# Optimization experiments

Hardware: AMD Instinct MI355X
Metric: run time of the kernel (lower is better)

## Reference

```python
import jax, jax.numpy as jnp
import numpy as np

B = 1024          # global batch
D = 512           # embedding_size
C = 100000        # num_classes (sum over 8 shards)
S = 64.0          # ArcFace scale
M = 0.5           # ArcFace additive angular margin
EPS = 1e-30


def setup_inputs() -> dict:
    key = jax.random.key(0)
    k1, k2, k3 = jax.random.split(key, 3)
    embeddings = jax.random.normal(k1, (B, D), dtype=jnp.float32)
    weight = jax.random.normal(k2, (C, D), dtype=jnp.float32)
    labels = jax.random.randint(k3, (B,), 0, C, dtype=jnp.int64)
    return {"embeddings": embeddings, "weight": weight, "labels": labels}


def reference(embeddings, weight, labels):
    # normalize(embeddings), normalize(weight) -> cosine logits
    ne = embeddings * jax.lax.rsqrt(jnp.sum(embeddings * embeddings, axis=1, keepdims=True))
    nw = weight * jax.lax.rsqrt(jnp.sum(weight * weight, axis=1, keepdims=True))
    logits = jnp.clip(jnp.einsum("bd,cd->bc", ne, nw), -1.0, 1.0)  # [B, C]

    rows = jnp.arange(B)
    target_logit = logits[rows, labels]
    # ArcFace: cos(theta + m), theta+m clipped to pi (insightface CombinedMarginLoss m2)
    theta = jnp.arccos(jnp.clip(target_logit, -1.0, 1.0))
    new_target = jnp.cos(jnp.minimum(theta + M, jnp.float32(np.pi)))
    logits = logits.at[rows, labels].set(new_target) * S

    # FusedDistCrossEntropy (single-device equivalent): stable softmax,
    # gather target prob, loss = -mean(log(clamp(p_target, 1e-30)))
    logp = jax.nn.log_softmax(logits, axis=1)
    p_target = jnp.exp(logp[rows, labels])
    loss = -jnp.mean(jnp.log(jnp.maximum(p_target, EPS)))
    return loss
```

## Files before the change

kernel.cpp:

```cpp
#include <hip/hip_runtime.h>
#include <hip/hip_bf16.h>
#include <math.h>
#include <stdint.h>

#define B_BATCH   1024
#define D_DIM     512
#define C_CLASSES 100000
#define BM        128
#define BN        128
#define BK        64
#define KITERS    (D_DIM / BK)
#define MTILES    (B_BATCH / BM)
#define NTILES    ((C_CLASSES + BN - 1) / BN)
#define NGROUPS   98
#define GRID_G    (8 * 8 * NGROUPS)
#define WBLK      (C_CLASSES / 8)
#define ABLK      (B_BATCH / 8)
#define LOG2E     1.44269504088896340736f
#define COSM      0.87758256189037276f
#define SINM      0.47942553860420301f
#define NEG_LOG_EPS 69.07755278982137f

typedef short bf16x8 __attribute__((ext_vector_type(8)));
typedef float f32x4  __attribute__((ext_vector_type(4)));

static __device__ __forceinline__ unsigned short f2bf(float f) {
    unsigned int u = __builtin_bit_cast(unsigned int, f);
    u += 0x7fffu + ((u >> 16) & 1u);
    return (unsigned short)(u >> 16);
}

static __device__ __forceinline__ unsigned int pk_rne(float lo, float hi) {
    return (unsigned int)f2bf(lo) | ((unsigned int)f2bf(hi) << 16);
}

static __device__ __forceinline__ unsigned int pk_bf16_trunc(float lo, float hi) {
    return __builtin_amdgcn_perm(__builtin_bit_cast(unsigned int, hi),
                                 __builtin_bit_cast(unsigned int, lo),
                                 0x07060302u);
}

static __device__ __forceinline__ void gld16(const unsigned short* g, unsigned short* l) {
    __builtin_amdgcn_global_load_lds(
        (const __attribute__((address_space(1))) unsigned int*)g,
        (__attribute__((address_space(3))) unsigned int*)l, 16, 0, 0);
}

__global__ __launch_bounds__(256) void prep(const float* __restrict__ W,
                                            const float* __restrict__ E,
                                            unsigned short* __restrict__ Wbf,
                                            unsigned short* __restrict__ Abf,
                                            float* __restrict__ out) {
    const int blk  = blockIdx.x;
    const int wave = threadIdx.x >> 6;
    const int lane = threadIdx.x & 63;
    const bool isW = blk < WBLK;
    if (!isW && blk == WBLK && threadIdx.x == 0) *out = 0.f;

    const float* src = isW ? W : E;
    unsigned short* dst = isW ? Wbf : Abf;
    const int r0 = (isW ? blk : blk - WBLK) * 8 + wave * 2;
    const int r1 = r0 + 1;

    const float4* s0 = (const float4*)(src + (size_t)r0 * D_DIM);
    const float4* s1 = (const float4*)(src + (size_t)r1 * D_DIM);
    float4 a0 = s0[2 * lane], a1 = s0[2 * lane + 1];
    float4 b0 = s1[2 * lane], b1 = s1[2 * lane + 1];

    float sa = a0.x*a0.x + a0.y*a0.y + a0.z*a0.z + a0.w*a0.w
             + a1.x*a1.x + a1.y*a1.y + a1.z*a1.z + a1.w*a1.w;
    float sb = b0.x*b0.x + b0.y*b0.y + b0.z*b0.z + b0.w*b0.w
             + b1.x*b1.x + b1.y*b1.y + b1.z*b1.z + b1.w*b1.w;
    #pragma unroll
    for (int off = 1; off < 64; off <<= 1) {
        sa += __shfl_xor(sa, off);
        sb += __shfl_xor(sb, off);
    }
    float ia = rsqrtf(sa), ib = rsqrtf(sb);
    a0.x *= ia; a0.y *= ia; a0.z *= ia; a0.w *= ia;
    a1.x *= ia; a1.y *= ia; a1.z *= ia; a1.w *= ia;
    b0.x *= ib; b0.y *= ib; b0.z *= ib; b0.w *= ib;
    b1.x *= ib; b1.y *= ib; b1.z *= ib; b1.w *= ib;

    uint4 oa, ob;
    if (isW) {
        oa = (uint4){pk_bf16_trunc(a0.x, a0.y), pk_bf16_trunc(a0.z, a0.w),
                     pk_bf16_trunc(a1.x, a1.y), pk_bf16_trunc(a1.z, a1.w)};
        ob = (uint4){pk_bf16_trunc(b0.x, b0.y), pk_bf16_trunc(b0.z, b0.w),
                     pk_bf16_trunc(b1.x, b1.y), pk_bf16_trunc(b1.z, b1.w)};
    } else {
        oa = (uint4){pk_rne(a0.x, a0.y), pk_rne(a0.z, a0.w),
                     pk_rne(a1.x, a1.y), pk_rne(a1.z, a1.w)};
        ob = (uint4){pk_rne(b0.x, b0.y), pk_rne(b0.z, b0.w),
                     pk_rne(b1.x, b1.y), pk_rne(b1.z, b1.w)};
    }
    ((uint4*)(dst + (size_t)r0 * D_DIM))[lane] = oa;
    ((uint4*)(dst + (size_t)r1 * D_DIM))[lane] = ob;
}

static __device__ __forceinline__ float epi_term(float accv, int col, int lab,
                                                 float* __restrict__ st, int srow) {
    float c = fminf(1.f, fmaxf(-1.f, accv));
    if (col >= C_CLASSES) return 0.f;
    float s = c * 64.0f;
    if (col == lab) {
        float sn = sqrtf(fmaxf(0.f, 1.f - c * c));
        float nm = c * COSM - sn * SINM;
        if (c < -COSM) nm = -1.f;
        s = nm * 64.0f;
        st[srow] = s;
    }
    return exp2f((s - 64.0f) * LOG2E);
}

__global__ __launch_bounds__(256, 4) void gemm_cos(const unsigned short* __restrict__ Abf,
                                                   const unsigned short* __restrict__ Wbf,
                                                   const int* __restrict__ labels,
                                                   float* __restrict__ st,
                                                   float* __restrict__ partial) {
    __shared__ unsigned short As[BM * BK];
    __shared__ unsigned short Bs[BN * BK];
    __shared__ float rowSum[BM];
    __shared__ int   labs[BM];

    const int id = blockIdx.x;
    const int x  = id & 7;
    const int s  = id >> 3;
    const int mt = s & 7;
    const int y  = x + 8 * (s >> 3);
    if (y >= NTILES) return;
    const int m0 = mt * BM;
    const int n0 = y * BN;

    const int tid = threadIdx.x;
    if (tid < BM) { labs[tid] = labels[m0 + tid]; rowSum[tid] = 0.f; }

    const int lane = tid & 63;
    const int wave = tid >> 6;
    const int wm = wave & 1, wn = wave >> 1;
    const int l15 = lane & 15, quad = lane >> 4;

    const int rIn = lane >> 3;
    const int csl = (((lane & 7) ^ rIn) << 4);
    const char* gA[4];
    const char* gB[4];
    unsigned short* lA[4];
    unsigned short* lB[4];
    #pragma unroll
    for (int c = 0; c < 4; ++c) {
        const int chunk = wave * 4 + c;
        const int row = chunk * 8 + rIn;
        gA[c] = (const char*)Abf + (size_t)(m0 + row) * (D_DIM * 2) + csl;
        const int bRow = min(n0 + row, C_CLASSES - 1);
        gB[c] = (const char*)Wbf + (size_t)bRow * (D_DIM * 2) + csl;
        lA[c] = &As[chunk * 512];
        lB[c] = &Bs[chunk * 512];
    }

    const f32x4 z = (f32x4){0.f, 0.f, 0.f, 0.f};
    f32x4 a00 = z, a01 = z, a02 = z, a03 = z;
    f32x4 a10 = z, a11 = z, a12 = z, a13 = z;
    f32x4 a20 = z, a21 = z, a22 = z, a23 = z;
    f32x4 a30 = z, a31 = z, a32 = z, a33 = z;

    const char* baseA = (const char*)As + (size_t)(wm * 64 + l15) * 128;
    const char* baseB = (const char*)Bs + (size_t)(wn * 64 + l15) * 128;
    const int q0 = ((quad ^ (l15 & 7)) << 4);

    for (int kk = 0; kk < KITERS; ++kk) {
        __syncthreads();
        #pragma unroll
        for (int c = 0; c < 4; ++c) {
            gld16((const unsigned short*)gA[c], lA[c]); gA[c] += 2 * BK;
            gld16((const unsigned short*)gB[c], lB[c]); gB[c] += 2 * BK;
        }
        __syncthreads();

        #pragma unroll
        for (int kh = 0; kh < 2; ++kh) {
            const int off = q0 ^ (kh << 6);
            bf16x8 af0 = *(const bf16x8*)(baseA          + off);
            bf16x8 af1 = *(const bf16x8*)(baseA + 2048   + off);
            bf16x8 af2 = *(const bf16x8*)(baseA + 4096   + off);
            bf16x8 af3 = *(const bf16x8*)(baseA + 6144   + off);
            bf16x8 bf0 = *(const bf16x8*)(baseB          + off);
            bf16x8 bf1 = *(const bf16x8*)(baseB + 2048   + off);
            bf16x8 bf2 = *(const bf16x8*)(baseB + 4096   + off);
            bf16x8 bf3 = *(const bf16x8*)(baseB + 6144   + off);

            a00 = __builtin_amdgcn_mfma_f32_16x16x32_bf16(af0, bf0, a00, 0, 0, 0);
            a01 = __builtin_amdgcn_mfma_f32_16x16x32_bf16(af0, bf1, a01, 0, 0, 0);
            a02 = __builtin_amdgcn_mfma_f32_16x16x32_bf16(af0, bf2, a02, 0, 0, 0);
            a03 = __builtin_amdgcn_mfma_f32_16x16x32_bf16(af0, bf3, a03, 0, 0, 0);
            a10 = __builtin_amdgcn_mfma_f32_16x16x32_bf16(af1, bf0, a10, 0, 0, 0);
            a11 = __builtin_amdgcn_mfma_f32_16x16x32_bf16(af1, bf1, a11, 0, 0, 0);
            a12 = __builtin_amdgcn_mfma_f32_16x16x32_bf16(af1, bf2, a12, 0, 0, 0);
            a13 = __builtin_amdgcn_mfma_f32_16x16x32_bf16(af1, bf3, a13, 0, 0, 0);
            a20 = __builtin_amdgcn_mfma_f32_16x16x32_bf16(af2, bf0, a20, 0, 0, 0);
            a21 = __builtin_amdgcn_mfma_f32_16x16x32_bf16(af2, bf1, a21, 0, 0, 0);
            a22 = __builtin_amdgcn_mfma_f32_16x16x32_bf16(af2, bf2, a22, 0, 0, 0);
            a23 = __builtin_amdgcn_mfma_f32_16x16x32_bf16(af2, bf3, a23, 0, 0, 0);
            a30 = __builtin_amdgcn_mfma_f32_16x16x32_bf16(af3, bf0, a30, 0, 0, 0);
            a31 = __builtin_amdgcn_mfma_f32_16x16x32_bf16(af3, bf1, a31, 0, 0, 0);
            a32 = __builtin_amdgcn_mfma_f32_16x16x32_bf16(af3, bf2, a32, 0, 0, 0);
            a33 = __builtin_amdgcn_mfma_f32_16x16x32_bf16(af3, bf3, a33, 0, 0, 0);
        }
    }

    const int colbase = n0 + wn * 64 + l15;

    #define EPIROW(A0, A1, A2, A3, MI)                                         \
    {                                                                          \
        _Pragma("unroll")                                                      \
        for (int r = 0; r < 4; ++r) {                                          \
            const int rloc = wm * 64 + (MI) * 16 + quad * 4 + r;               \
            const int lab = labs[rloc];                                        \
            float part = 0.f;                                                  \
            part += epi_term((A0)[r], colbase,      lab, st, m0 + rloc);       \
            part += epi_term((A1)[r], colbase + 16, lab, st, m0 + rloc);       \
            part += epi_term((A2)[r], colbase + 32, lab, st, m0 + rloc);       \
            part += epi_term((A3)[r], colbase + 48, lab, st, m0 + rloc);       \
            part += __shfl_xor(part, 1);                                       \
            part += __shfl_xor(part, 2);                                       \
            part += __shfl_xor(part, 4);                                       \
            part += __shfl_xor(part, 8);                                       \
            if (l15 == 0) atomicAdd(&rowSum[rloc], part);                      \
        }                                                                      \
    }

    EPIROW(a00, a01, a02, a03, 0)
    EPIROW(a10, a11, a12, a13, 1)
    EPIROW(a20, a21, a22, a23, 2)
    EPIROW(a30, a31, a32, a33, 3)
    #undef EPIROW

    __syncthreads();
    if (tid < BM) partial[(size_t)(m0 + tid) * NTILES + y] = rowSum[tid];
}

__global__ __launch_bounds__(64) void reduce_loss(const float* __restrict__ partial,
                                                  const float* __restrict__ st,
                                                  float* __restrict__ out) {
    const int b = blockIdx.x;
    const int l = threadIdx.x;
    const float* row = partial + (size_t)b * NTILES;
    float L = 0.f;
    for (int t = l; t < NTILES; t += 64) L += row[t];
    #pragma unroll
    for (int off = 1; off < 64; off <<= 1) L += __shfl_xor(L, off);
    if (l == 0) {
        float logp = st[b] - 64.0f - logf(L);
        float lossb = fminf(-logp, NEG_LOG_EPS) * (1.0f / (float)B_BATCH);
        atomicAdd(out, lossb);
    }
}

extern "C" void kernel_launch(void* const* d_in, const int* in_sizes, int n_in,
                              void* d_out, int out_size, void* d_ws, size_t ws_size,
                              hipStream_t stream) {
    const float* emb = (const float*)d_in[0];
    const float* wgt = (const float*)d_in[1];
    const int*   lab = (const int*)d_in[2];
    float* out = (float*)d_out;
    char* ws = (char*)d_ws;

    const size_t WBF_B = (size_t)C_CLASSES * D_DIM * 2;
    const size_t ABF_B = (size_t)B_BATCH * D_DIM * 2;

    unsigned short* Wbf = (unsigned short*)ws;
    unsigned short* Abf = (unsigned short*)(ws + WBF_B);
    float* st      = (float*)(ws + WBF_B + ABF_B);
    float* partial = (float*)(ws + WBF_B + ABF_B + 4096);

    prep<<<WBLK + ABLK, 256, 0, stream>>>(wgt, emb, Wbf, Abf, out);
    gemm_cos<<<GRID_G, 256, 0, stream>>>(Abf, Wbf, lab, st, partial);
    reduce_loss<<<B_BATCH, 64, 0, stream>>>(partial, st, out);
}
```

Before: 459.1 us.

## Triple-buffer GEMM with 256x128 tiles, 512 threads, interleaved staging and setprio

Switches the cosine GEMM to 256x128 tiles with 8 waves per block and a three-stage LDS ring. Global-to-LDS loads for tile k+2 are interleaved between MFMA phases, with barriers and s_setprio around each phase. The block-to-XCD mapping is remapped, and the epilogue uses a cheaper exp (fma plus clamp) with an edge-check template so full tiles skip bounds tests. The goal is to hide load latency and cut the redundant W-tile loads per row of A. The cost is more LDS and registers, lower occupancy, and many barriers.

```diff
diff --git a/kernel.cpp b/kernel.cpp
--- a/kernel.cpp
+++ b/kernel.cpp
@@ -6,23 +6,27 @@
 #define B_BATCH   1024
 #define D_DIM     512
 #define C_CLASSES 100000
-#define BM        128
+#define BM        256
 #define BN        128
 #define BK        64
-#define KITERS    (D_DIM / BK)
-#define MTILES    (B_BATCH / BM)
+#define KT        (D_DIM / BK)
+#define MT        (B_BATCH / BM)
 #define NTILES    ((C_CLASSES + BN - 1) / BN)
-#define NGROUPS   98
-#define GRID_G    (8 * 8 * NGROUPS)
+#define GRID_G    (MT * NTILES)
+#define CPX       (GRID_G / 8)
 #define WBLK      (C_CLASSES / 8)
 #define ABLK      (B_BATCH / 8)
 #define LOG2E     1.44269504088896340736f
+#define K64LOG2E  92.33248261689366f
 #define COSM      0.87758256189037276f
 #define SINM      0.47942553860420301f
 #define NEG_LOG_EPS 69.07755278982137f
 
 typedef short bf16x8 __attribute__((ext_vector_type(8)));
 typedef float f32x4  __attribute__((ext_vector_type(4)));
+
+#define FENCE asm volatile("" ::: "memory")
+#define BAR() do { FENCE; __builtin_amdgcn_s_barrier(); FENCE; } while (0)
 
 static __device__ __forceinline__ unsigned short f2bf(float f) {
     unsigned int u = __builtin_bit_cast(unsigned int, f);
@@ -40,7 +44,7 @@
                                  0x07060302u);
 }
 
-static __device__ __forceinline__ void gld16(const unsigned short* g, unsigned short* l) {
+static __device__ __forceinline__ void gld16(const void* g, const unsigned short* l) {
     __builtin_amdgcn_global_load_lds(
         (const __attribute__((address_space(1))) unsigned int*)g,
         (__attribute__((address_space(3))) unsigned int*)l, 16, 0, 0);
@@ -98,144 +102,183 @@
     ((uint4*)(dst + (size_t)r1 * D_DIM))[lane] = ob;
 }
 
+template<bool EDGE>
 static __device__ __forceinline__ float epi_term(float accv, int col, int lab,
                                                  float* __restrict__ st, int srow) {
-    float c = fminf(1.f, fmaxf(-1.f, accv));
-    if (col >= C_CLASSES) return 0.f;
-    float s = c * 64.0f;
+    if (EDGE && col >= C_CLASSES) return 0.f;
+    float t = exp2f(fminf(0.f, __builtin_fmaf(accv, K64LOG2E, -K64LOG2E)));
     if (col == lab) {
+        float c = fminf(1.f, fmaxf(-1.f, accv));
         float sn = sqrtf(fmaxf(0.f, 1.f - c * c));
         float nm = c * COSM - sn * SINM;
         if (c < -COSM) nm = -1.f;
-        s = nm * 64.0f;
+        float s = nm * 64.0f;
         st[srow] = s;
-    }
-    return exp2f((s - 64.0f) * LOG2E);
-}
-
-__global__ __launch_bounds__(256, 4) void gemm_cos(const unsigned short* __restrict__ Abf,
+        t = exp2f((s - 64.0f) * LOG2E);
+    }
+    return t;
+}
+
+__global__ __launch_bounds__(512, 2) void gemm_cos(const unsigned short* __restrict__ Abf,
                                                    const unsigned short* __restrict__ Wbf,
                                                    const int* __restrict__ labels,
                                                    float* __restrict__ st,
                                                    float* __restrict__ partial) {
-    __shared__ unsigned short As[BM * BK];
-    __shared__ unsigned short Bs[BN * BK];
+    __shared__ unsigned short sA[3][BM * BK];
+    __shared__ unsigned short sB[3][BN * BK];
     __shared__ float rowSum[BM];
     __shared__ int   labs[BM];
 
-    const int id = blockIdx.x;
-    const int x  = id & 7;
-    const int s  = id >> 3;
-    const int mt = s & 7;
-    const int y  = x + 8 * (s >> 3);
-    if (y >= NTILES) return;
+    const int wg = (blockIdx.x & 7) * CPX + (blockIdx.x >> 3);
+    const int mt = wg & 3;
+    const int nt = wg >> 2;
     const int m0 = mt * BM;
-    const int n0 = y * BN;
-
-    const int tid = threadIdx.x;
-    if (tid < BM) { labs[tid] = labels[m0 + tid]; rowSum[tid] = 0.f; }
-
+    const int n0 = nt * BN;
+
+    const int tid  = threadIdx.x;
     const int lane = tid & 63;
     const int wave = tid >> 6;
-    const int wm = wave & 1, wn = wave >> 1;
-    const int l15 = lane & 15, quad = lane >> 4;
-
-    const int rIn = lane >> 3;
-    const int csl = (((lane & 7) ^ rIn) << 4);
+    const int wm   = wave & 1;
+    const int wn   = wave >> 1;
+    const int l15  = lane & 15, quad = lane >> 4;
+
+    if (tid < BM) { labs[tid] = labels[m0 + tid]; rowSum[tid] = 0.f; }
+
+    const int rIn   = lane >> 3;
+    const int scolb = (((lane & 7) ^ rIn) << 4);
     const char* gA[4];
-    const char* gB[4];
-    unsigned short* lA[4];
-    unsigned short* lB[4];
-    #pragma unroll
-    for (int c = 0; c < 4; ++c) {
-        const int chunk = wave * 4 + c;
-        const int row = chunk * 8 + rIn;
-        gA[c] = (const char*)Abf + (size_t)(m0 + row) * (D_DIM * 2) + csl;
-        const int bRow = min(n0 + row, C_CLASSES - 1);
-        gB[c] = (const char*)Wbf + (size_t)bRow * (D_DIM * 2) + csl;
-        lA[c] = &As[chunk * 512];
-        lB[c] = &Bs[chunk * 512];
+    const char* gB[2];
+    int lAo[4], lBo[2];
+    #pragma unroll
+    for (int i = 0; i < 4; ++i) {
+        const int chunk = wave * 4 + i;
+        gA[i]  = (const char*)Abf + (size_t)(m0 + chunk * 8 + rIn) * (D_DIM * 2) + scolb;
+        lAo[i] = chunk * 512;
+    }
+    #pragma unroll
+    for (int i = 0; i < 2; ++i) {
+        const int chunk = wave * 2 + i;
+        const int bRow  = min(n0 + chunk * 8 + rIn, C_CLASSES - 1);
+        gB[i]  = (const char*)Wbf + (size_t)bRow * (D_DIM * 2) + scolb;
+        lBo[i] = chunk * 512;
+    }
+
+    #pragma unroll
+    for (int tt = 0; tt < 2; ++tt) {
+        #pragma unroll
+        for (int i = 0; i < 4; ++i) gld16(gA[i] + tt * 128, &sA[tt][lAo[i]]);
+        #pragma unroll
+        for (int i = 0; i < 2; ++i) gld16(gB[i] + tt * 128, &sB[tt][lBo[i]]);
     }
 
     const f32x4 z = (f32x4){0.f, 0.f, 0.f, 0.f};
-    f32x4 a00 = z, a01 = z, a02 = z, a03 = z;
-    f32x4 a10 = z, a11 = z, a12 = z, a13 = z;
-    f32x4 a20 = z, a21 = z, a22 = z, a23 = z;
-    f32x4 a30 = z, a31 = z, a32 = z, a33 = z;
-
-    const char* baseA = (const char*)As + (size_t)(wm * 64 + l15) * 128;
-    const char* baseB = (const char*)Bs + (size_t)(wn * 64 + l15) * 128;
+    f32x4 acc[8][2];
+    #pragma unroll
+    for (int m = 0; m < 8; ++m) { acc[m][0] = z; acc[m][1] = z; }
+
     const int q0 = ((quad ^ (l15 & 7)) << 4);
 
-    for (int kk = 0; kk < KITERS; ++kk) {
-        __syncthreads();
-        #pragma unroll
-        for (int c = 0; c < 4; ++c) {
-            gld16((const unsigned short*)gA[c], lA[c]); gA[c] += 2 * BK;
-            gld16((const unsigned short*)gB[c], lB[c]); gB[c] += 2 * BK;
+    #define MFMA2(MA, AF)                                                          \
+        _Pragma("unroll")                                                          \
+        for (int n = 0; n < 2; ++n) {                                              \
+            acc[MA][n] = __builtin_amdgcn_mfma_f32_16x16x32_bf16((AF)[0], bfr[n][0], acc[MA][n], 0, 0, 0); \
+            acc[MA][n] = __builtin_amdgcn_mfma_f32_16x16x32_bf16((AF)[1], bfr[n][1], acc[MA][n], 0, 0, 0); \
         }
-        __syncthreads();
-
-        #pragma unroll
-        for (int kh = 0; kh < 2; ++kh) {
-            const int off = q0 ^ (kh << 6);
-            bf16x8 af0 = *(const bf16x8*)(baseA          + off);
-            bf16x8 af1 = *(const bf16x8*)(baseA + 2048   + off);
-            bf16x8 af2 = *(const bf16x8*)(baseA + 4096   + off);
-            bf16x8 af3 = *(const bf16x8*)(baseA + 6144   + off);
-            bf16x8 bf0 = *(const bf16x8*)(baseB          + off);
-            bf16x8 bf1 = *(const bf16x8*)(baseB + 2048   + off);
-            bf16x8 bf2 = *(const bf16x8*)(baseB + 4096   + off);
-            bf16x8 bf3 = *(const bf16x8*)(baseB + 6144   + off);
-
-            a00 = __builtin_amdgcn_mfma_f32_16x16x32_bf16(af0, bf0, a00, 0, 0, 0);
-            a01 = __builtin_amdgcn_mfma_f32_16x16x32_bf16(af0, bf1, a01, 0, 0, 0);
-            a02 = __builtin_amdgcn_mfma_f32_16x16x32_bf16(af0, bf2, a02, 0, 0, 0);
-            a03 = __builtin_amdgcn_mfma_f32_16x16x32_bf16(af0, bf3, a03, 0, 0, 0);
-            a10 = __builtin_amdgcn_mfma_f32_16x16x32_bf16(af1, bf0, a10, 0, 0, 0);
-            a11 = __builtin_amdgcn_mfma_f32_16x16x32_bf16(af1, bf1, a11, 0, 0, 0);
-            a12 = __builtin_amdgcn_mfma_f32_16x16x32_bf16(af1, bf2, a12, 0, 0, 0);
-            a13 = __builtin_amdgcn_mfma_f32_16x16x32_bf16(af1, bf3, a13, 0, 0, 0);
-            a20 = __builtin_amdgcn_mfma_f32_16x16x32_bf16(af2, bf0, a20, 0, 0, 0);
-            a21 = __builtin_amdgcn_mfma_f32_16x16x32_bf16(af2, bf1, a21, 0, 0, 0);
-            a22 = __builtin_amdgcn_mfma_f32_16x16x32_bf16(af2, bf2, a22, 0, 0, 0);
-            a23 = __builtin_amdgcn_mfma_f32_16x16x32_bf16(af2, bf3, a23, 0, 0, 0);
-            a30 = __builtin_amdgcn_mfma_f32_16x16x32_bf16(af3, bf0, a30, 0, 0, 0);
-            a31 = __builtin_amdgcn_mfma_f32_16x16x32_bf16(af3, bf1, a31, 0, 0, 0);
-            a32 = __builtin_amdgcn_mfma_f32_16x16x32_bf16(af3, bf2, a32, 0, 0, 0);
-            a33 = __builtin_amdgcn_mfma_f32_16x16x32_bf16(af3, bf3, a33, 0, 0, 0);
+
+    #define KTILE(T, CUR, STG, WAITN, DOSTAGE)                                     \
+    {                                                                              \
+        asm volatile("s_waitcnt vmcnt(" #WAITN ")" ::: "memory");                  \
+        BAR();                                                                     \
+        const char* aB = (const char*)&sA[CUR][0] + (size_t)(wm * 128 + l15) * 128;\
+        const char* bB = (const char*)&sB[CUR][0] + (size_t)(wn * 32  + l15) * 128;\
+        bf16x8 bfr[2][2], af0[2], af1[2];                                          \
+                  \
+        _Pragma("unroll")                                                          \
+        for (int kh = 0; kh < 2; ++kh) {                                           \
+            bfr[0][kh] = *(const bf16x8*)(bB          + (q0 ^ (kh << 6)));         \
+            bfr[1][kh] = *(const bf16x8*)(bB + 2048   + (q0 ^ (kh << 6)));         \
+            af0[kh]    = *(const bf16x8*)(aB          + (q0 ^ (kh << 6)));         \
+            af1[kh]    = *(const bf16x8*)(aB + 2048   + (q0 ^ (kh << 6)));         \
+        }                                                                          \
+        if (DOSTAGE) { gld16(gA[0] + (T + 2) * 128, &sA[STG][lAo[0]]);             \
+                       gld16(gA[1] + (T + 2) * 128, &sA[STG][lAo[1]]); }           \
+        BAR();                                                                     \
+        __builtin_amdgcn_s_setprio(1);                                             \
+        MFMA2(0, af0) MFMA2(1, af1)                                                \
+        __builtin_amdgcn_s_setprio(0);                                             \
+        BAR();                                                                     \
+                                         \
+        _Pragma("unroll")                                                          \
+        for (int kh = 0; kh < 2; ++kh) {                                           \
+            af0[kh] = *(const bf16x8*)(aB + 4096 + (q0 ^ (kh << 6)));              \
+            af1[kh] = *(const bf16x8*)(aB + 6144 + (q0 ^ (kh << 6)));              \
+        }                                                                          \
+        if (DOSTAGE) { gld16(gA[2] + (T + 2) * 128, &sA[STG][lAo[2]]);             \
+                       gld16(gA[3] + (T + 2) * 128, &sA[STG][lAo[3]]); }           \
+        BAR();                                                                     \
+        __builtin_amdgcn_s_setprio(1);                                             \
+        MFMA2(2, af0) MFMA2(3, af1)                                                \
+        __builtin_amdgcn_s_setprio(0);                                             \
+        BAR();                                                                     \
+                                         \
+        _Pragma("unroll")                                                          \
+        for (int kh = 0; kh < 2; ++kh) {                                           \
+            af0[kh] = *(const bf16x8*)(aB +  8192 + (q0 ^ (kh << 6)));             \
+            af1[kh] = *(const bf16x8*)(aB + 10240 + (q0 ^ (kh << 6)));             \
+        }                                                                          \
+        if (DOSTAGE) { gld16(gB[0] + (T + 2) * 128, &sB[STG][lBo[0]]);             \
+                       gld16(gB[1] + (T + 2) * 128, &sB[STG][lBo[1]]); }           \
+        BAR();                                                                     \
+        __builtin_amdgcn_s_setprio(1);                                             \
+        MFMA2(4, af0) MFMA2(5, af1)                                                \
+        __builtin_amdgcn_s_setprio(0);                                             \
+        BAR();                                                                     \
+                                                              \
+        _Pragma("unroll")                                                          \
+        for (int kh = 0; kh < 2; ++kh) {                                           \
+            af0[kh] = *(const bf16x8*)(aB + 12288 + (q0 ^ (kh << 6)));             \
+            af1[kh] = *(const bf16x8*)(aB + 14336 + (q0 ^ (kh << 6)));             \
+        }                                                                          \
+        BAR();                                                                     \
+        __builtin_amdgcn_s_setprio(1);                                             \
+        MFMA2(6, af0) MFMA2(7, af1)                                                \
+        __builtin_amdgcn_s_setprio(0);                                             \
+        BAR();                                                                     \
+    }
+
+    KTILE(0, 0, 2, 6, true)
+    KTILE(1, 1, 0, 6, true)
+    KTILE(2, 2, 1, 6, true)
+    KTILE(3, 0, 2, 6, true)
+    KTILE(4, 1, 0, 6, true)
+    KTILE(5, 2, 1, 6, true)
+    KTILE(6, 0, 2, 6, false)
+    KTILE(7, 1, 0, 0, false)
+    #undef KTILE
+    #undef MFMA2
+
+    const int colbase = n0 + wn * 32 + l15;
+    #define EPI(EDGE)                                                              \
+        _Pragma("unroll")                                                          \
+        for (int m = 0; m < 8; ++m) {                                              \
+            _Pragma("unroll")                                                      \
+            for (int r = 0; r < 4; ++r) {                                          \
+                const int rloc = wm * 128 + m * 16 + quad * 4 + r;                 \
+                const int lab = labs[rloc];                                        \
+                float part = epi_term<EDGE>(acc[m][0][r], colbase,      lab, st, m0 + rloc) \
+                           + epi_term<EDGE>(acc[m][1][r], colbase + 16, lab, st, m0 + rloc);\
+                part += __shfl_xor(part, 1);                                       \
+                part += __shfl_xor(part, 2);                                       \
+                part += __shfl_xor(part, 4);                                       \
+                part += __shfl_xor(part, 8);                                       \
+                if (l15 == 0) atomicAdd(&rowSum[rloc], part);                      \
+            }                                                                      \
         }
-    }
-
-    const int colbase = n0 + wn * 64 + l15;
-
-    #define EPIROW(A0, A1, A2, A3, MI)                                         \
-    {                                                                          \
-        _Pragma("unroll")                                                      \
-        for (int r = 0; r < 4; ++r) {                                          \
-            const int rloc = wm * 64 + (MI) * 16 + quad * 4 + r;               \
-            const int lab = labs[rloc];                                        \
-            float part = 0.f;                                                  \
-            part += epi_term((A0)[r], colbase,      lab, st, m0 + rloc);       \
-            part += epi_term((A1)[r], colbase + 16, lab, st, m0 + rloc);       \
-            part += epi_term((A2)[r], colbase + 32, lab, st, m0 + rloc);       \
-            part += epi_term((A3)[r], colbase + 48, lab, st, m0 + rloc);       \
-            part += __shfl_xor(part, 1);                                       \
-            part += __shfl_xor(part, 2);                                       \
-            part += __shfl_xor(part, 4);                                       \
-            part += __shfl_xor(part, 8);                                       \
-            if (l15 == 0) atomicAdd(&rowSum[rloc], part);                      \
-        }                                                                      \
-    }
-
-    EPIROW(a00, a01, a02, a03, 0)
-    EPIROW(a10, a11, a12, a13, 1)
-    EPIROW(a20, a21, a22, a23, 2)
-    EPIROW(a30, a31, a32, a33, 3)
-    #undef EPIROW
+    if (n0 + BN <= C_CLASSES) { EPI(false) } else { EPI(true) }
+    #undef EPI
 
     __syncthreads();
-    if (tid < BM) partial[(size_t)(m0 + tid) * NTILES + y] = rowSum[tid];
+    if (tid < BM) partial[(size_t)(m0 + tid) * NTILES + nt] = rowSum[tid];
 }
 
 __global__ __launch_bounds__(64) void reduce_loss(const float* __restrict__ partial,
@@ -273,6 +316,6 @@
     float* partial = (float*)(ws + WBF_B + ABF_B + 4096);
 
     prep<<<WBLK + ABLK, 256, 0, stream>>>(wgt, emb, Wbf, Abf, out);
-    gemm_cos<<<GRID_G, 256, 0, stream>>>(Abf, Wbf, lab, st, partial);
+    gemm_cos<<<GRID_G, 512, 0, stream>>>(Abf, Wbf, lab, st, partial);
     reduce_loss<<<B_BATCH, 64, 0, stream>>>(partial, st, out);
 }
```

New measurement: 539.8 us. 1.18x slower.
